# Kernel tuning notes

Hardware: AMD Instinct MI355X
Metric: run time of the kernel (lower is better)

Reference implementation:

```python
import jax, jax.numpy as jnp
import numpy as np

CH, XH, YH, RADIUS = 2, 2, 2, 1  # channel_heads, x_heads, y_heads, neighborhood radius


def neighborhood_mask(n_sub_x, n_sub_y, radius):
    # clamped neighbor offsets reduce to |di|<=r and |dj|<=r within the grid
    iy = jnp.arange(n_sub_y)
    ix = jnp.arange(n_sub_x)
    my = jnp.abs(iy[:, None] - iy[None, :]) <= radius  # [ny, ny]
    mx = jnp.abs(ix[:, None] - ix[None, :]) <= radius  # [nx, nx]
    m = my[:, None, :, None] & mx[None, :, None, :]    # [ny, nx, ny, nx]
    s = n_sub_x * n_sub_y
    return m.reshape(s, s)  # row-major (h1 w1)(h2 w2), matching einops


def setup_inputs() -> dict:
    key = jax.random.key(0)
    k1, k2, k3 = jax.random.split(key, 3)
    C = 128
    seq = jax.random.normal(k1, (2, 256, C, 16, 16), dtype=jnp.float32)
    w_qkv = jax.random.normal(k2, (3 * C, C), dtype=jnp.float32) / np.sqrt(C).astype(np.float32)
    w_out = jax.random.normal(k3, (C, C), dtype=jnp.float32) / np.sqrt(C).astype(np.float32)
    b_out = jnp.zeros((C,), dtype=jnp.float32)
    return {"seq": seq, "w_qkv": w_qkv, "w_out": w_out, "b_out": b_out,
            "n_sub_x": 16, "n_sub_y": 16}


def reference(seq, w_qkv, w_out, b_out, n_sub_x, n_sub_y):
    b, s, C, H, W = seq.shape
    h, w = H // YH, W // XH
    c = C // CH
    nH = YH * XH * CH  # total heads

    # pointwise qkv projection over channels: [b, s, 3C, H, W]
    qkv = jnp.einsum('bschw,dc->bsdhw', seq, w_qkv)

    # decompose2d: split spatial grid into y_heads x x_heads blocks -> spatial heads
    # [b, s, 3C, YH, h, XH, w] -> [b, s, YH*XH, 3C, h, w]
    qkv = qkv.reshape(b, s, 3 * C, YH, h, XH, w)
    qkv = qkv.transpose(0, 1, 3, 5, 2, 4, 6).reshape(b, s, YH * XH, 3 * C, h, w)

    # split into q,k,v and channel heads: 3C = 3 * CH * c
    qkv = qkv.reshape(b, s, YH * XH, 3, CH, c, h, w)
    # -> [3, b, (spatial_heads * channel_heads), s, c, h, w]
    qkv = qkv.transpose(3, 0, 2, 4, 1, 5, 6, 7).reshape(3, b, nH, s, c, h, w)
    q, k, v = qkv[0], qkv[1], qkv[2]

    # scaled dot-product attention over flattened function dim (c,h,w)
    scale = 1.0 / np.sqrt(c * h * w).astype(np.float32)
    scores = jnp.einsum('bnschw,bntchw->bnst', q, k) * scale  # [b, nH, s, s]
    mask = neighborhood_mask(n_sub_x, n_sub_y, RADIUS)  # [s, s]
    scores = jnp.where(mask[None, None, :, :], scores, jnp.finfo(scores.dtype).min)
    attn = jax.nn.softmax(scores, axis=-1)
    sa = jnp.einsum('bnst,bntchw->bnschw', attn, v)  # [b, nH, s, c, h, w]

    # merge channel heads back: [b, s, spatial_heads, C, h, w]
    sa = sa.reshape(b, YH * XH, CH, s, c, h, w)
    sa = sa.transpose(0, 3, 1, 2, 4, 5, 6).reshape(b, s, YH, XH, C, h, w)
    # recompose2d: [b, s, C, H, W]
    sa = sa.transpose(0, 1, 4, 2, 5, 3, 6).reshape(b, s, C, H, W)

    # output pointwise projection with bias
    out = jnp.einsum('bschw,dc->bsdhw', sa, w_out) + b_out[None, None, :, None, None]
    return out
```

## Files before the change

### kernel.cpp

```cpp
#include <hip/hip_runtime.h>

#define BATCH 2
#define SS    256
#define CC    128
#define HWN   256
#define FDIM  4096

typedef unsigned int uint;
typedef unsigned short ushort;
typedef short bf16x8 __attribute__((ext_vector_type(8)));
typedef ushort us4 __attribute__((ext_vector_type(4)));
typedef float f32x4 __attribute__((ext_vector_type(4)));

__device__ __forceinline__ ushort f2b(float f) {
  uint u = __float_as_uint(f);
  return (ushort)((u + 0x7fffu + ((u >> 16) & 1u)) >> 16);
}
__device__ __forceinline__ float b2f(ushort h) { return __uint_as_float((uint)h << 16); }

__global__ void k_convert(const float* __restrict__ wqkv, const float* __restrict__ wout,
                          ushort* __restrict__ wqkv_b, ushort* __restrict__ wout_b) {
  int i = blockIdx.x * 256 + threadIdx.x;
  if (i < 384 * 128) wqkv_b[i] = f2b(wqkv[i]);
  if (i < 128 * 128) {
    const int cc = i & 127;
    const int ks = cc >> 5, qq = (cc >> 3) & 3, j = cc & 7;
    const int creal = (ks >> 1) * 64 + ((((ks & 1) << 1) | (qq >> 1)) << 4)
                      + ((qq & 1) << 3) + j;
    wout_b[i] = f2b(wout[(i >> 7) * 128 + creal]);
  }
}

__global__ __launch_bounds__(256, 2) void k_qkv(const float* __restrict__ seq,
                                                const ushort* __restrict__ wqkv_b,
                                                ushort* __restrict__ qkvh) {
  __shared__ ushort wlds[128 * 128];
  const int bs = blockIdx.x;
  const int b = bs >> 8, s = bs & 255;
  const int t = threadIdx.x;
  const int hq = t >> 6, lane = t & 63;
  const int qq = lane >> 4, m = lane & 15;

  const float* sp = seq + (size_t)bs * (CC * HWN);

  bf16x8 bfrag[4][4];
  uint obase[4];
  #pragma unroll
  for (int set = 0; set < 4; ++set) {
    const int ntg = hq * 4 + set;
    const int hw = ntg * 16 + m;
    #pragma unroll
    for (int ks = 0; ks < 4; ++ks) {
      const int k0 = ks * 32 + qq * 8;
      float tmp[8];
      #pragma unroll
      for (int j = 0; j < 8; ++j) tmp[j] = sp[(k0 + j) * HWN + hw];
      bf16x8 fr;
      #pragma unroll
      for (int j = 0; j < 8; ++j) fr[j] = (short)f2b(tmp[j]);
      bfrag[set][ks] = fr;
    }
    const int n_qk = ((ntg >> 3) * 2 + (m >> 3)) * 2;
    const int hwl  = (ntg & 7) * 8 + (m & 7);
    obase[set] = (uint)(((b * 8 + n_qk) * SS + s) * FDIM + hwl * 16 + qq * 4);
  }

  for (int qkvi = 0; qkvi < 3; ++qkvi) {
    if (qkvi) __syncthreads();
    #pragma unroll
    for (int i = 0; i < 8; ++i) {
      const int row = i * 16 + (t >> 4), col16 = t & 15;
      bf16x8 w = *(const bf16x8*)(wqkv_b + (qkvi * 128 + row) * 128 + col16 * 8);
      *(bf16x8*)&wlds[row * 128 + ((col16 ^ (row & 15)) * 8)] = w;
    }
    __syncthreads();

    #pragma unroll
    for (int mt8 = 0; mt8 < 8; ++mt8) {
      bf16x8 afrag[4];
      #pragma unroll
      for (int ks = 0; ks < 4; ++ks)
        afrag[ks] = *(const bf16x8*)&wlds[(mt8 * 16 + m) * 128 + (((ks * 4 + qq) ^ m) * 8)];
      const int ch = mt8 >> 2, m4 = mt8 & 3;
      #pragma unroll
      for (int set = 0; set < 4; ++set) {
        f32x4 acc = {0.f, 0.f, 0.f, 0.f};
        #pragma unroll
        for (int ks = 0; ks < 4; ++ks)
          acc = __builtin_amdgcn_mfma_f32_16x16x32_bf16(afrag[ks], bfrag[set][ks], acc, 0, 0, 0);
        us4 pk;
        #pragma unroll
        for (int r = 0; r < 4; ++r) pk[r] = f2b(acc[r]);
        *(us4*)(qkvh + obase[set]
                + (uint)((qkvi * 16 + ch) * (SS * FDIM) + m4 * 1024)) = pk;
      }
    }
  }
}

__global__ __launch_bounds__(1024) void k_scores(const ushort* __restrict__ qkvh,
                                                 float* __restrict__ attn) {
  __shared__ float red[16][64][12];
  const int g = blockIdx.x;
  const int unit = (g & 7) * 32 + (g >> 3);
  const int b  = unit >> 7;
  const int n  = (unit >> 4) & 7;
  const int sy = unit & 15;
  const int t = threadIdx.x;
  const int wave = t >> 6, lane = t & 63;
  const int qq = lane >> 4, l15 = lane & 15;
  const size_t hs = (size_t)SS * FDIM;
  const ushort* qb = qkvh + (size_t)(b * 8 + n) * hs;
  const ushort* kb = qkvh + (size_t)(16 + b * 8 + n) * hs;

  const ushort* qp = qb + (size_t)(sy * 16 + l15) * FDIM + qq * 8;
  const ushort* kp[3];
  #pragma unroll
  for (int tl = 0; tl < 3; ++tl) {
    const int tyc = min(max(sy - 1 + tl, 0), 15);
    kp[tl] = kb + (size_t)(tyc * 16 + l15) * FDIM + qq * 8;
  }

  f32x4 acc[3] = {{0,0,0,0},{0,0,0,0},{0,0,0,0}};
  const int kbeg = wave * 256;
  #pragma unroll
  for (int it = 0; it < 4; ++it) {
    const int k0 = kbeg + it * 64;
    bf16x8 a0 = *(const bf16x8*)(qp + k0);
    bf16x8 a1 = *(const bf16x8*)(qp + k0 + 32);
    bf16x8 b0[3], b1[3];
    #pragma unroll
    for (int tl = 0; tl < 3; ++tl) {
      b0[tl] = *(const bf16x8*)(kp[tl] + k0);
      b1[tl] = *(const bf16x8*)(kp[tl] + k0 + 32);
    }
    #pragma unroll
    for (int tl = 0; tl < 3; ++tl)
      acc[tl] = __builtin_amdgcn_mfma_f32_16x16x32_bf16(a0, b0[tl], acc[tl], 0, 0, 0);
    #pragma unroll
    for (int tl = 0; tl < 3; ++tl)
      acc[tl] = __builtin_amdgcn_mfma_f32_16x16x32_bf16(a1, b1[tl], acc[tl], 0, 0, 0);
  }

  #pragma unroll
  for (int tl = 0; tl < 3; ++tl)
    #pragma unroll
    for (int r = 0; r < 4; ++r) red[wave][lane][tl * 4 + r] = acc[tl][r];
  __syncthreads();
  if (t < 768) {
    const int lane2 = t / 12, idx = t - lane2 * 12;
    float ssum = red[0][lane2][idx];
    #pragma unroll
    for (int w = 1; w < 16; ++w) ssum += red[w][lane2][idx];
    red[0][lane2][idx] = ssum;
  }
  __syncthreads();
  if (wave != 0) return;
  #pragma unroll
  for (int tl = 0; tl < 3; ++tl)
    #pragma unroll
    for (int r = 0; r < 4; ++r) acc[tl][r] = red[0][lane][tl * 4 + r];

  const int tx = l15;
  float sc[3][4];
  #pragma unroll
  for (int tl = 0; tl < 3; ++tl) {
    const int ty = sy - 1 + tl;
    const bool tyv = (ty >= 0 && ty < 16);
    #pragma unroll
    for (int r = 0; r < 4; ++r) {
      const int sx = qq * 4 + r;
      const bool v = tyv && (tx - sx <= 1) && (sx - tx <= 1);
      sc[tl][r] = v ? acc[tl][r] * (1.f / 64.f) : -1e30f;
    }
  }
  #pragma unroll
  for (int r = 0; r < 4; ++r) {
    float mx = fmaxf(fmaxf(sc[0][r], sc[1][r]), sc[2][r]);
    #pragma unroll
    for (int off = 1; off < 16; off <<= 1) mx = fmaxf(mx, __shfl_xor(mx, off));
    float p[3], sum = 0.f;
    #pragma unroll
    for (int tl = 0; tl < 3; ++tl) { p[tl] = __expf(sc[tl][r] - mx); sum += p[tl]; }
    #pragma unroll
    for (int off = 1; off < 16; off <<= 1) sum += __shfl_xor(sum, off);
    const float inv = 1.f / sum;
    const int sx = qq * 4 + r;
    const int s = sy * 16 + sx;
    #pragma unroll
    for (int tl = 0; tl < 3; ++tl) {
      const int ty = sy - 1 + tl;
      const int dxp = tx - sx + 1;
      if (ty >= 0 && ty < 16 && dxp >= 0 && dxp <= 2)
        attn[((size_t)(b * 8 + n) * SS + s) * 9 + tl * 3 + dxp] = p[tl] * inv;
    }
  }
}

__global__ __launch_bounds__(256) void k_pv(const ushort* __restrict__ qkvh,
                                            const float* __restrict__ attn,
                                            ushort* __restrict__ sa) {
  const int g = blockIdx.x;
  const int unit = (g & 7) * 512 + (g >> 3);
  const int eta = unit >> 8, s = unit & 255;
  const int sy = s >> 4, sx = s & 15;
  const int t = threadIdx.x;
  const size_t hs = (size_t)SS * FDIM;

  float p[9];
  int sjc[9];
  bool vld[9];
  #pragma unroll
  for (int j = 0; j < 9; ++j) {
    const int ny = sy + j / 3 - 1, nx = sx + j % 3 - 1;
    vld[j] = (ny >= 0 && ny < 16 && nx >= 0 && nx < 16);
    sjc[j] = min(max(ny, 0), 15) * 16 + min(max(nx, 0), 15);
    p[j] = vld[j] ? attn[((size_t)eta * SS + s) * 9 + j] : 0.f;
  }

  const ushort* vb = qkvh + (size_t)(32 + eta) * hs;
  const int f0 = t * 16;
  float acc[16];
  #pragma unroll
  for (int e = 0; e < 16; ++e) acc[e] = 0.f;
  #pragma unroll
  for (int j = 0; j < 9; ++j) {
    if (vld[j]) {
      const ushort* vp = vb + (size_t)sjc[j] * FDIM + f0;
      bf16x8 v0 = *(const bf16x8*)(vp);
      bf16x8 v1 = *(const bf16x8*)(vp + 8);
      const float pj = p[j];
      #pragma unroll
      for (int e = 0; e < 8; ++e) acc[e]     += pj * b2f((ushort)v0[e]);
      #pragma unroll
      for (int e = 0; e < 8; ++e) acc[8 + e] += pj * b2f((ushort)v1[e]);
    }
  }
  bf16x8 r0, r1;
  #pragma unroll
  for (int e = 0; e < 8; ++e) { r0[e] = (short)f2b(acc[e]); r1[e] = (short)f2b(acc[8 + e]); }
  ushort* op = sa + ((size_t)eta * SS + s) * FDIM + f0;
  *(bf16x8*)op = r0;
  *(bf16x8*)(op + 8) = r1;
}

__global__ __launch_bounds__(256) void k_proj(const ushort* __restrict__ qkvh,
                                              const ushort* __restrict__ wout_b,
                                              const float* __restrict__ bout,
                                              float* __restrict__ out) {
  __shared__ ushort wlds[128 * 128];
  const int g = blockIdx.x;
  const int r9 = g >> 3;
  const int G = (g & 7) * 4 + (r9 >> 6);
  const int idx = r9 & 63;
  const int b = G >> 4, sy = G & 15;
  const int sx = idx >> 2, sub = idx & 3;
  const int s = sy * 16 + sx;
  const int bs = b * 256 + s;
  const int t = threadIdx.x;
  const int wave = t >> 6, lane = t & 63;
  const int ntg = sub * 4 + wave;
  const int qq = lane >> 4, m = lane & 15;
  const size_t hs = (size_t)SS * FDIM;

  #pragma unroll
  for (int i = 0; i < 8; ++i) {
    const int row = i * 16 + (t >> 4), col16 = t & 15;
    bf16x8 w = *(const bf16x8*)(wout_b + row * 128 + col16 * 8);
    *(bf16x8*)&wlds[row * 128 + ((col16 ^ (row & 15)) * 8)] = w;
  }

  const int nbase = ((ntg >> 3) * 2 + (m >> 3)) * 2;
  const int hwl = (ntg & 7) * 8 + (m & 7);
  bf16x8 bfrag[4];
  #pragma unroll
  for (int ks = 0; ks < 4; ++ks) {
    const int ch = ks >> 1;
    const int c64hi = ((ks & 1) << 1) | (qq >> 1);
    const int half = qq & 1;
    const ushort* sb = qkvh + (size_t)(b * 8 + nbase + ch) * hs;
    const int off = c64hi * 1024 + hwl * 16 + half * 8;
    bfrag[ks] = *(const bf16x8*)(sb + (size_t)s * FDIM + off);
  }

  __syncthreads();

  #pragma unroll
  for (int mt = 0; mt < 8; ++mt) {
    bf16x8 afrag[4];
    #pragma unroll
    for (int ks = 0; ks < 4; ++ks)
      afrag[ks] = *(const bf16x8*)&wlds[(mt * 16 + m) * 128 + (((ks * 4 + qq) ^ m) * 8)];
    f32x4 acc = {0.f, 0.f, 0.f, 0.f};
    #pragma unroll
    for (int ks = 0; ks < 4; ++ks)
      acc = __builtin_amdgcn_mfma_f32_16x16x32_bf16(afrag[ks], bfrag[ks], acc, 0, 0, 0);
    const int hw = ntg * 16 + m;
    #pragma unroll
    for (int r = 0; r < 4; ++r) {
      const int d = mt * 16 + qq * 4 + r;
      out[((size_t)bs * CC + d) * HWN + hw] = acc[r] + bout[d];
    }
  }
}

extern "C" void kernel_launch(void* const* d_in, const int* in_sizes, int n_in,
                              void* d_out, int out_size, void* d_ws, size_t ws_size,
                              hipStream_t stream) {
  const float* seq  = (const float*)d_in[0];
  const float* wqkv = (const float*)d_in[1];
  const float* wout = (const float*)d_in[2];
  const float* bout = (const float*)d_in[3];
  char* ws = (char*)d_ws;
  ushort* wqkv_b = (ushort*)(ws);
  ushort* wout_b = (ushort*)(ws + 98304);
  ushort* qkvh   = (ushort*)(ws + 131072);
  float*  attn   = (float*)(ws + 131072 + 100663296ull);
  float*  outp   = (float*)d_out;

  hipLaunchKernelGGL(k_convert, dim3(192),  dim3(256), 0, stream, wqkv, wout, wqkv_b, wout_b);
  hipLaunchKernelGGL(k_qkv,     dim3(512),  dim3(256), 0, stream, seq, wqkv_b, qkvh);
  hipLaunchKernelGGL(k_scores,  dim3(256),  dim3(1024), 0, stream, qkvh, attn);
  hipLaunchKernelGGL(k_pv,      dim3(4096), dim3(256), 0, stream, qkvh, attn, qkvh );
  hipLaunchKernelGGL(k_proj,    dim3(2048), dim3(256), 0, stream, qkvh, wout_b, bout, outp);
}
```

Measured before the change: 195.2 us.

## Fuse weight bf16 conversion into qkv/proj kernels and widen qkv blocks

Removes the separate weight-conversion kernel launch and converts the fp32 weights to bf16 on the fly while staging them into LDS in k_qkv and k_proj, including the column permutation for w_out. k_qkv also moves from 256 to 512 threads per block, so each wave handles two column groups instead of four, which lowers register pressure and raises occupancy. The cost is that every block now reads twice as many weight bytes (fp32) and repeats the conversion arithmetic, in exchange for one fewer launch and better latency hiding in k_qkv.

```diff
diff --git a/kernel.cpp b/kernel.cpp
--- a/kernel.cpp
+++ b/kernel.cpp
@@ -18,36 +18,23 @@
 }
 __device__ __forceinline__ float b2f(ushort h) { return __uint_as_float((uint)h << 16); }
 
-__global__ void k_convert(const float* __restrict__ wqkv, const float* __restrict__ wout,
-                          ushort* __restrict__ wqkv_b, ushort* __restrict__ wout_b) {
-  int i = blockIdx.x * 256 + threadIdx.x;
-  if (i < 384 * 128) wqkv_b[i] = f2b(wqkv[i]);
-  if (i < 128 * 128) {
-    const int cc = i & 127;
-    const int ks = cc >> 5, qq = (cc >> 3) & 3, j = cc & 7;
-    const int creal = (ks >> 1) * 64 + ((((ks & 1) << 1) | (qq >> 1)) << 4)
-                      + ((qq & 1) << 3) + j;
-    wout_b[i] = f2b(wout[(i >> 7) * 128 + creal]);
-  }
-}
-
-__global__ __launch_bounds__(256, 2) void k_qkv(const float* __restrict__ seq,
-                                                const ushort* __restrict__ wqkv_b,
+__global__ __launch_bounds__(512, 4) void k_qkv(const float* __restrict__ seq,
+                                                const float* __restrict__ wqkv,
                                                 ushort* __restrict__ qkvh) {
   __shared__ ushort wlds[128 * 128];
   const int bs = blockIdx.x;
   const int b = bs >> 8, s = bs & 255;
   const int t = threadIdx.x;
-  const int hq = t >> 6, lane = t & 63;
+  const int wv = t >> 6, lane = t & 63;
   const int qq = lane >> 4, m = lane & 15;
 
   const float* sp = seq + (size_t)bs * (CC * HWN);
 
-  bf16x8 bfrag[4][4];
-  uint obase[4];
-  #pragma unroll
-  for (int set = 0; set < 4; ++set) {
-    const int ntg = hq * 4 + set;
+  bf16x8 bfrag[2][4];
+  uint obase[2];
+  #pragma unroll
+  for (int set = 0; set < 2; ++set) {
+    const int ntg = wv * 2 + set;
     const int hw = ntg * 16 + m;
     #pragma unroll
     for (int ks = 0; ks < 4; ++ks) {
@@ -68,10 +55,15 @@
   for (int qkvi = 0; qkvi < 3; ++qkvi) {
     if (qkvi) __syncthreads();
     #pragma unroll
-    for (int i = 0; i < 8; ++i) {
-      const int row = i * 16 + (t >> 4), col16 = t & 15;
-      bf16x8 w = *(const bf16x8*)(wqkv_b + (qkvi * 128 + row) * 128 + col16 * 8);
-      *(bf16x8*)&wlds[row * 128 + ((col16 ^ (row & 15)) * 8)] = w;
+    for (int i = 0; i < 4; ++i) {
+      const int row = i * 32 + (t >> 4), col16 = t & 15;
+      const float* wp = wqkv + (size_t)(qkvi * 128 + row) * 128 + col16 * 8;
+      f32x4 w0 = *(const f32x4*)(wp);
+      f32x4 w1 = *(const f32x4*)(wp + 4);
+      bf16x8 fr;
+      #pragma unroll
+      for (int e = 0; e < 4; ++e) { fr[e] = (short)f2b(w0[e]); fr[4 + e] = (short)f2b(w1[e]); }
+      *(bf16x8*)&wlds[row * 128 + ((col16 ^ (row & 15)) * 8)] = fr;
     }
     __syncthreads();
 
@@ -83,7 +75,7 @@
         afrag[ks] = *(const bf16x8*)&wlds[(mt8 * 16 + m) * 128 + (((ks * 4 + qq) ^ m) * 8)];
       const int ch = mt8 >> 2, m4 = mt8 & 3;
       #pragma unroll
-      for (int set = 0; set < 4; ++set) {
+      for (int set = 0; set < 2; ++set) {
         f32x4 acc = {0.f, 0.f, 0.f, 0.f};
         #pragma unroll
         for (int ks = 0; ks < 4; ++ks)
@@ -245,7 +237,7 @@
 }
 
 __global__ __launch_bounds__(256) void k_proj(const ushort* __restrict__ qkvh,
-                                              const ushort* __restrict__ wout_b,
+                                              const float* __restrict__ wout,
                                               const float* __restrict__ bout,
                                               float* __restrict__ out) {
   __shared__ ushort wlds[128 * 128];
@@ -263,11 +255,22 @@
   const int qq = lane >> 4, m = lane & 15;
   const size_t hs = (size_t)SS * FDIM;
 
-  #pragma unroll
-  for (int i = 0; i < 8; ++i) {
-    const int row = i * 16 + (t >> 4), col16 = t & 15;
-    bf16x8 w = *(const bf16x8*)(wout_b + row * 128 + col16 * 8);
-    *(bf16x8*)&wlds[row * 128 + ((col16 ^ (row & 15)) * 8)] = w;
+  {
+    const int col16 = t & 15;
+    const int ks = col16 >> 2, qw = col16 & 3;
+    const int creal0 = (ks >> 1) * 64 + ((((ks & 1) << 1) | (qw >> 1)) << 4)
+                       + ((qw & 1) << 3);
+    #pragma unroll
+    for (int i = 0; i < 8; ++i) {
+      const int row = i * 16 + (t >> 4);
+      const float* wp = wout + (size_t)row * 128 + creal0;
+      f32x4 w0 = *(const f32x4*)(wp);
+      f32x4 w1 = *(const f32x4*)(wp + 4);
+      bf16x8 fr;
+      #pragma unroll
+      for (int e = 0; e < 4; ++e) { fr[e] = (short)f2b(w0[e]); fr[4 + e] = (short)f2b(w1[e]); }
+      *(bf16x8*)&wlds[row * 128 + ((col16 ^ (row & 15)) * 8)] = fr;
+    }
   }
 
   const int nbase = ((ntg >> 3) * 2 + (m >> 3)) * 2;
@@ -312,15 +315,12 @@
   const float* wout = (const float*)d_in[2];
   const float* bout = (const float*)d_in[3];
   char* ws = (char*)d_ws;
-  ushort* wqkv_b = (ushort*)(ws);
-  ushort* wout_b = (ushort*)(ws + 98304);
-  ushort* qkvh   = (ushort*)(ws + 131072);
-  float*  attn   = (float*)(ws + 131072 + 100663296ull);
-  float*  outp   = (float*)d_out;
-
-  hipLaunchKernelGGL(k_convert, dim3(192),  dim3(256), 0, stream, wqkv, wout, wqkv_b, wout_b);
-  hipLaunchKernelGGL(k_qkv,     dim3(512),  dim3(256), 0, stream, seq, wqkv_b, qkvh);
-  hipLaunchKernelGGL(k_scores,  dim3(256),  dim3(1024), 0, stream, qkvh, attn);
-  hipLaunchKernelGGL(k_pv,      dim3(4096), dim3(256), 0, stream, qkvh, attn, qkvh );
-  hipLaunchKernelGGL(k_proj,    dim3(2048), dim3(256), 0, stream, qkvh, wout_b, bout, outp);
-}
+  ushort* qkvh = (ushort*)(ws);
+  float*  attn = (float*)(ws + 100663296ull);
+  float*  outp = (float*)d_out;
+
+  hipLaunchKernelGGL(k_qkv,    dim3(512),  dim3(512),  0, stream, seq, wqkv, qkvh);
+  hipLaunchKernelGGL(k_scores, dim3(256),  dim3(1024), 0, stream, qkvh, attn);
+  hipLaunchKernelGGL(k_pv,     dim3(4096), dim3(256),  0, stream, qkvh, attn, qkvh );
+  hipLaunchKernelGGL(k_proj,   dim3(2048), dim3(256),  0, stream, qkvh, wout, bout, outp);
+}
```

After: 195.2 us. No clear change (+0.0%).
